# Kernel optimization log

Hardware: AMD Instinct MI355X
Metric: run time of the kernel (lower is better)

Reference implementation:

```python
import jax, jax.numpy as jnp
import numpy as np

S, B, DIM = 1024, 4, 768
N_EXPERTS = 8
# hidden_dim = 256 * ceil(int(2*4*dim/3)/256) = 2048 for dim=768
HID = 2048


def setup_inputs() -> dict:
    key = jax.random.key(0)
    ks = jax.random.split(key, 6)
    scale = 0.02
    return {
        "hidden_states": jax.random.normal(ks[0], (S, B, DIM), dtype=jnp.float32),
        "router_w": jax.random.normal(ks[1], (DIM, N_EXPERTS), dtype=jnp.float32) * scale,
        "router_b": jnp.zeros((N_EXPERTS,), dtype=jnp.float32),
        "w1": jax.random.normal(ks[2], (N_EXPERTS, DIM, HID), dtype=jnp.float32) * scale,
        "w2": jax.random.normal(ks[3], (N_EXPERTS, DIM, HID), dtype=jnp.float32) * scale,
        "w3": jax.random.normal(ks[4], (N_EXPERTS, HID, DIM), dtype=jnp.float32) * scale,
    }


def reference(hidden_states, router_w, router_b, w1, w2, w3):
    s, b, h = hidden_states.shape
    # top-1 router
    route = jax.nn.softmax(hidden_states @ router_w + router_b, axis=2)  # [s,b,E]
    max_prob = jnp.max(route, axis=2).reshape(-1, 1)   # [T,1]
    max_ind = jnp.argmax(route, axis=2).reshape(-1)    # [T]
    x = hidden_states.reshape(-1, h)                   # [T,d]

    out = jnp.zeros_like(x)
    # fixed small loop over experts; masked dispatch (tokens not routed to e
    # are zeroed so they contribute nothing)
    for e in range(N_EXPERTS):
        mask = (max_ind == e)[:, None]                 # [T,1]
        xe = jnp.where(mask, x, 0.0)
        oe = (jax.nn.silu(xe @ w1[e]) * (xe @ w2[e])) @ w3[e]
        out = out + jnp.where(mask, oe, 0.0)

    # original stores expert outputs in a bf16 buffer before the prob combine
    out = out.astype(jnp.bfloat16) * max_prob          # bf16 * f32 -> f32
    return out.reshape(s, b, h)
```

## Files before the change

kernel.cpp:

```cpp
#include <hip/hip_runtime.h>


#define T_TOK 4096
#define DIM   768
#define HID   2048
#define NE    8
#define ECAP  1024

#define KB1 24
#define NB1 128
#define KB2 64
#define NB2 48
#define MBC 64

typedef _Float16 f16x8 __attribute__((ext_vector_type(8)));
typedef float    f32x4 __attribute__((ext_vector_type(4)));

__device__ __forceinline__ float bf16_rne(float v) {
    unsigned u = __float_as_uint(v);
    unsigned r = (u + 0x7fffu + ((u >> 16) & 1u)) & 0xffff0000u;
    return __uint_as_float(r);
}

__global__ void moe_init_kernel(int* __restrict__ counts) {
    if (threadIdx.x < NE) counts[threadIdx.x] = 0;
}

__device__ __forceinline__ void convert_tile(
    const float* __restrict__ src, _Float16* __restrict__ dst,
    float* Lt, int N, int KBc, int ngrp, int kgrp)
{
    const int t  = threadIdx.x;
    const int c4 = (t & 31) * 4;
    const int r0 = (t >> 5) * 8;
    const float* p = src + (size_t)(kgrp * 64 + r0) * N + ngrp * 128 + c4;
    float4 v[8];
#pragma unroll
    for (int j = 0; j < 8; ++j) v[j] = *(const float4*)(p + (size_t)j * N);
#pragma unroll
    for (int j = 0; j < 8; ++j) {
        float* row = &Lt[(r0 + j) * 130 + c4];
        *(float2*)(row)     = make_float2(v[j].x, v[j].y);
        *(float2*)(row + 2) = make_float2(v[j].z, v[j].w);
    }
    __syncthreads();

    const int l = t & 63, w = t >> 6;
    const int fr = l & 15, fq = l >> 4;
#pragma unroll
    for (int i = 0; i < 4; ++i) {
        const int cell = w * 4 + i;
        const int kbl = cell >> 3, nbl = cell & 7;
        f16x8 h;
#pragma unroll
        for (int j = 0; j < 8; ++j)
            h[j] = (_Float16)Lt[(kbl * 32 + fq * 8 + j) * 130 + nbl * 16 + fr];
        const int nb = ngrp * 8 + nbl, kb = kgrp * 2 + kbl;
        *(f16x8*)(dst + ((size_t)nb * KBc + kb) * 512 + l * 8) = h;
    }
}

__global__ __launch_bounds__(256) void moe_convert_w1_kernel(
    const float* __restrict__ w1, _Float16* __restrict__ w1s)
{
    __shared__ float Lt[64 * 130];
    const int e = blockIdx.x / 192, tile = blockIdx.x % 192;
    convert_tile(w1 + (size_t)e * DIM * HID, w1s + (size_t)e * NB1 * KB1 * 512,
                 Lt, HID, KB1, tile & 15, tile >> 4);
}

__global__ __launch_bounds__(256) void moe_convert_w2_kernel(
    const float* __restrict__ w2, _Float16* __restrict__ w2s)
{
    __shared__ float Lt[64 * 130];
    const int e = blockIdx.x / 192, tile = blockIdx.x % 192;
    convert_tile(w2 + (size_t)e * DIM * HID, w2s + (size_t)e * NB1 * KB1 * 512,
                 Lt, HID, KB1, tile & 15, tile >> 4);
}

__global__ __launch_bounds__(256) void moe_convert_w3_kernel(
    const float* __restrict__ w3, _Float16* __restrict__ w3s)
{
    __shared__ float Lt[64 * 130];
    const int e = blockIdx.x / 192, tile = blockIdx.x % 192;
    convert_tile(w3 + (size_t)e * HID * DIM, w3s + (size_t)e * NB2 * KB2 * 512,
                 Lt, DIM, KB2, tile % 6, tile / 6);
}

__global__ __launch_bounds__(256) void moe_router_kernel(
    const float* __restrict__ X, const float* __restrict__ rw,
    const float* __restrict__ rb, float* __restrict__ probs,
    int* __restrict__ counts, int* __restrict__ lists)
{
    const int t    = blockIdx.x * 4 + (threadIdx.x >> 6);
    const int lane = threadIdx.x & 63;
    const float* x = X + (size_t)t * DIM;

    float xv[12];
#pragma unroll
    for (int j = 0; j < 12; ++j) xv[j] = x[lane + j * 64];

    double lg[NE];
#pragma unroll
    for (int e = 0; e < NE; ++e) {
        double s = 0.0;
#pragma unroll
        for (int j = 0; j < 12; ++j)
            s += (double)xv[j] * (double)rw[(lane + j * 64) * NE + e];
#pragma unroll
        for (int off = 32; off >= 1; off >>= 1) s += __shfl_xor(s, off, 64);
        lg[e] = s + (double)rb[e];
    }

    if (lane == 0) {
        double m = lg[0]; int mi = 0;
#pragma unroll
        for (int e = 1; e < NE; ++e)
            if (lg[e] > m) { m = lg[e]; mi = e; }
        float sum = 0.f;
#pragma unroll
        for (int e = 0; e < NE; ++e) sum += expf((float)(lg[e] - m));
        probs[t] = 1.0f / sum;
        int pos = atomicAdd(&counts[mi], 1);
        lists[mi * T_TOK + pos] = t;
    }
}

__global__ __launch_bounds__(256) void moe_gather_kernel(
    const float* __restrict__ X, const int* __restrict__ lists,
    const int* __restrict__ counts, _Float16* __restrict__ Ag)
{
    const int e = blockIdx.z;
    int cnt = counts[e]; if (cnt > ECAP) cnt = ECAP;
    const int mgrp = blockIdx.y;
    if (mgrp * 64 >= ((cnt + 63) & ~63)) return;
    const int t = threadIdx.x, w = t >> 6, l = t & 63;
    const int mb = mgrp * 4 + w;
    const int m  = mb * 16 + (l & 15);
    const bool valid = (m < cnt);
    const int tok = valid ? lists[e * T_TOK + m] : 0;
    const float* xr = X + (size_t)tok * DIM + (l >> 4) * 8;
#pragma unroll
    for (int i = 0; i < 4; ++i) {
        const int kb = blockIdx.x * 4 + i;
        float4 a = make_float4(0.f, 0.f, 0.f, 0.f), b = a;
        if (valid) {
            a = *(const float4*)(xr + kb * 32);
            b = *(const float4*)(xr + kb * 32 + 4);
        }
        f16x8 h;
        h[0] = (_Float16)a.x; h[1] = (_Float16)a.y; h[2] = (_Float16)a.z; h[3] = (_Float16)a.w;
        h[4] = (_Float16)b.x; h[5] = (_Float16)b.y; h[6] = (_Float16)b.z; h[7] = (_Float16)b.w;
        *(f16x8*)(Ag + ((size_t)(e * MBC + mb) * KB1 + kb) * 512 + l * 8) = h;
    }
}

__global__ __launch_bounds__(256, 3) void moe_gemm1_kernel(
    const _Float16* __restrict__ Ag, const _Float16* __restrict__ w1s,
    const _Float16* __restrict__ w2s, const int* __restrict__ counts,
    _Float16* __restrict__ Hs)
{
    const int e = blockIdx.z;
    int cnt = counts[e]; if (cnt > ECAP) cnt = ECAP;
    const int by = blockIdx.y, bx = blockIdx.x;
    if (by * 128 >= cnt) return;
    const int t = threadIdx.x, w = t >> 6, l = t & 63;
    const int wm = w & 1, wn = w >> 1;

    __shared__ _Float16 Ls[2][16 * 512];
    __shared__ _Float16 Ep[4][64 * 40];

    const int c0s = w * 4;
    const _Float16* gsrc[4];
#pragma unroll
    for (int i = 0; i < 4; ++i) {
        const int c = c0s + i;
        if (c < 8)
            gsrc[i] = Ag  + ((size_t)((e * MBC + by * 8 + c) * KB1)) * 512;
        else if (c < 12)
            gsrc[i] = w1s + ((size_t)((e * NB1 + bx * 4 + (c - 8)) * KB1)) * 512;
        else
            gsrc[i] = w2s + ((size_t)((e * NB1 + bx * 4 + (c - 12)) * KB1)) * 512;
        gsrc[i] += (size_t)l * 8;
    }

    f32x4 acc1[4][2], acc2[4][2];
    const f32x4 zero = {0.f, 0.f, 0.f, 0.f};
#pragma unroll
    for (int i = 0; i < 4; ++i)
#pragma unroll
        for (int j = 0; j < 2; ++j) { acc1[i][j] = zero; acc2[i][j] = zero; }

    f16x8 st[4];
    auto G = [&](int kb) {
#pragma unroll
        for (int i = 0; i < 4; ++i)
            st[i] = *(const f16x8*)(gsrc[i] + (size_t)kb * 512);
    };

    G(0);
    for (int kb = 0; kb < KB1; ++kb) {
        _Float16* Lb = &Ls[kb & 1][0];
#pragma unroll
        for (int i = 0; i < 4; ++i)
            *(f16x8*)(Lb + (c0s + i) * 512 + l * 8) = st[i];
        __syncthreads();
        if (kb + 1 < KB1) G(kb + 1);

        f16x8 a[4], p[2], q[2];
#pragma unroll
        for (int i = 0; i < 4; ++i)
            a[i] = *(const f16x8*)(Lb + (wm * 4 + i) * 512 + l * 8);
#pragma unroll
        for (int j = 0; j < 2; ++j) {
            p[j] = *(const f16x8*)(Lb + (8  + wn * 2 + j) * 512 + l * 8);
            q[j] = *(const f16x8*)(Lb + (12 + wn * 2 + j) * 512 + l * 8);
        }
#pragma unroll
        for (int i = 0; i < 4; ++i)
#pragma unroll
            for (int j = 0; j < 2; ++j) {
                acc1[i][j] = __builtin_amdgcn_mfma_f32_16x16x32_f16(a[i], p[j], acc1[i][j], 0, 0, 0);
                acc2[i][j] = __builtin_amdgcn_mfma_f32_16x16x32_f16(a[i], q[j], acc2[i][j], 0, 0, 0);
            }
    }

    const int fq = l >> 4, fr = l & 15;
#pragma unroll
    for (int i = 0; i < 4; ++i)
#pragma unroll
        for (int j = 0; j < 2; ++j)
#pragma unroll
            for (int r = 0; r < 4; ++r) {
                const float h1 = acc1[i][j][r], h2 = acc2[i][j][r];
                const float s  = h1 / (1.f + __expf(-h1)) * h2;
                Ep[w][(i * 16 + fq * 4 + r) * 40 + j * 16 + fr] = (_Float16)s;
            }
    __syncthreads();
    const int kbH = bx * 2 + wn;
#pragma unroll
    for (int i = 0; i < 4; ++i) {
        f16x8 v = *(const f16x8*)&Ep[w][(i * 16 + fr) * 40 + fq * 8];
        *(f16x8*)(Hs + ((size_t)((e * MBC + by * 8 + wm * 4 + i) * KB2 + kbH)) * 512 + l * 8) = v;
    }
}

__global__ __launch_bounds__(256, 3) void moe_gemm2_kernel(
    const _Float16* __restrict__ Hs, const _Float16* __restrict__ w3s,
    const int* __restrict__ lists, const int* __restrict__ counts,
    const float* __restrict__ probs, float* __restrict__ out)
{
    const int e = blockIdx.z;
    int cnt = counts[e]; if (cnt > ECAP) cnt = ECAP;
    const int by = blockIdx.y, bx = blockIdx.x;
    if (by * 64 >= cnt) return;
    const int t = threadIdx.x, w = t >> 6, l = t & 63;

    __shared__ _Float16 La[2][8 * 512];

    const _Float16* Asrc = Hs + ((size_t)((e * MBC + by * 4 + w) * KB2)) * 512 + l * 8;
    const int nb0 = e * NB2 + bx * 8 + w * 2;
    const _Float16* Bb = w3s + ((size_t)nb0 * KB2) * 512 + l * 8;

    f32x4 acc[4][2];
    const f32x4 zero = {0.f, 0.f, 0.f, 0.f};
#pragma unroll
    for (int i = 0; i < 4; ++i) { acc[i][0] = zero; acc[i][1] = zero; }

    f16x8 stA[2];
    f16x8 vB0[4], vB1[4];

    auto GA = [&](int s) {
        stA[0] = *(const f16x8*)(Asrc + (size_t)(2 * s)     * 512);
        stA[1] = *(const f16x8*)(Asrc + (size_t)(2 * s + 1) * 512);
    };
    auto GB = [&](f16x8* vB, int s) {
#pragma unroll
        for (int u = 0; u < 2; ++u)
#pragma unroll
            for (int j = 0; j < 2; ++j)
                vB[u * 2 + j] = *(const f16x8*)(Bb + ((size_t)(j * KB2 + 2 * s + u)) * 512);
    };
    auto STEP = [&](int s, const f16x8* curB, f16x8* nxtB, _Float16* Lb) {
        *(f16x8*)(Lb +      w  * 512 + l * 8) = stA[0];
        *(f16x8*)(Lb + (4 + w) * 512 + l * 8) = stA[1];
        __syncthreads();
        if (s + 1 < KB2 / 2) { GA(s + 1); GB(nxtB, s + 1); }
#pragma unroll
        for (int u = 0; u < 2; ++u) {
            f16x8 a[4];
#pragma unroll
            for (int i = 0; i < 4; ++i)
                a[i] = *(const f16x8*)(Lb + (u * 4 + i) * 512 + l * 8);
#pragma unroll
            for (int i = 0; i < 4; ++i)
#pragma unroll
                for (int j = 0; j < 2; ++j)
                    acc[i][j] = __builtin_amdgcn_mfma_f32_16x16x32_f16(a[i], curB[u * 2 + j], acc[i][j], 0, 0, 0);
        }
    };

    GA(0); GB(vB0, 0);
    for (int s2 = 0; s2 < KB2 / 2; s2 += 2) {
        STEP(s2,     vB0, vB1, &La[0][0]);
        STEP(s2 + 1, vB1, vB0, &La[1][0]);
    }

    const int* list = lists + e * T_TOK;
    const int fq = l >> 4, fr = l & 15;
    const int c0 = bx * 128 + w * 32;
#pragma unroll
    for (int i = 0; i < 4; ++i)
#pragma unroll
        for (int r = 0; r < 4; ++r) {
            const int m = by * 64 + i * 16 + fq * 4 + r;
            if (m < cnt) {
                const int tok = list[m];
                const float pb = probs[tok];
                float* orow = out + (size_t)tok * DIM + c0 + fr;
                orow[0]  = bf16_rne(acc[i][0][r]) * pb;
                orow[16] = bf16_rne(acc[i][1][r]) * pb;
            }
        }
}

extern "C" void kernel_launch(void* const* d_in, const int* in_sizes, int n_in,
                              void* d_out, int out_size, void* d_ws, size_t ws_size,
                              hipStream_t stream) {
    const float* X  = (const float*)d_in[0];
    const float* rw = (const float*)d_in[1];
    const float* rb = (const float*)d_in[2];
    const float* w1 = (const float*)d_in[3];
    const float* w2 = (const float*)d_in[4];
    const float* w3 = (const float*)d_in[5];
    float* out = (float*)d_out;

    char* ws = (char*)d_ws;
    int*      counts = (int*)(ws + 0);
    int*      lists  = (int*)(ws + 256);
    float*    probs  = (float*)(ws + 131328);
    const size_t WSZ = 25165824;
    _Float16* w1s = (_Float16*)(ws + 147712);
    _Float16* w2s = (_Float16*)(ws + 147712 + WSZ);
    _Float16* w3s = (_Float16*)(ws + 147712 + 2 * WSZ);
    _Float16* Ag  = (_Float16*)(ws + 147712 + 3 * WSZ);
    _Float16* Hs  = (_Float16*)(ws + 147712 + 3 * WSZ + 12582912);

    hipLaunchKernelGGL(moe_init_kernel, dim3(1), dim3(64), 0, stream, counts);
    hipLaunchKernelGGL(moe_convert_w1_kernel, dim3(1536), dim3(256), 0, stream, w1, w1s);
    hipLaunchKernelGGL(moe_convert_w2_kernel, dim3(1536), dim3(256), 0, stream, w2, w2s);
    hipLaunchKernelGGL(moe_convert_w3_kernel, dim3(1536), dim3(256), 0, stream, w3, w3s);
    hipLaunchKernelGGL(moe_router_kernel, dim3(T_TOK / 4), dim3(256), 0, stream,
                       X, rw, rb, probs, counts, lists);
    hipLaunchKernelGGL(moe_gather_kernel, dim3(6, 16, 8), dim3(256), 0, stream,
                       X, lists, counts, Ag);
    hipLaunchKernelGGL(moe_gemm1_kernel, dim3(32, 8, 8), dim3(256), 0, stream,
                       Ag, w1s, w2s, counts, Hs);
    hipLaunchKernelGGL(moe_gemm2_kernel, dim3(6, 16, 8), dim3(256), 0, stream,
                       Hs, w3s, lists, counts, probs, out);
}
```

Before: 328.8 us.

## Split router into per-token argmax and deterministic ballot-based list build

The router now spreads each token's 8 expert dot products across lane groups, using float4 loads and shuffle reductions, and writes only the argmax index and probability. A new per-expert kernel builds token lists in token order using ballot and prefix counts, replacing the atomic append and the separate counts-init kernel. This removes atomic contention and makes list order deterministic, at the cost of one extra launch in which only 8 blocks serially scan all 4096 tokens. maxind reuses the Ag workspace before the gather overwrites it.

```diff
diff --git a/kernel.cpp b/kernel.cpp
--- a/kernel.cpp
+++ b/kernel.cpp
@@ -22,10 +22,6 @@
     return __uint_as_float(r);
 }
 
-__global__ void moe_init_kernel(int* __restrict__ counts) {
-    if (threadIdx.x < NE) counts[threadIdx.x] = 0;
-}
-
 __device__ __forceinline__ void convert_tile(
     const float* __restrict__ src, _Float16* __restrict__ dst,
     float* Lt, int N, int KBc, int ngrp, int kgrp)
@@ -90,40 +86,71 @@
 __global__ __launch_bounds__(256) void moe_router_kernel(
     const float* __restrict__ X, const float* __restrict__ rw,
     const float* __restrict__ rb, float* __restrict__ probs,
-    int* __restrict__ counts, int* __restrict__ lists)
-{
-    const int t    = blockIdx.x * 4 + (threadIdx.x >> 6);
-    const int lane = threadIdx.x & 63;
-    const float* x = X + (size_t)t * DIM;
-
-    float xv[12];
-#pragma unroll
-    for (int j = 0; j < 12; ++j) xv[j] = x[lane + j * 64];
-
-    double lg[NE];
-#pragma unroll
-    for (int e = 0; e < NE; ++e) {
-        double s = 0.0;
-#pragma unroll
-        for (int j = 0; j < 12; ++j)
-            s += (double)xv[j] * (double)rw[(lane + j * 64) * NE + e];
-#pragma unroll
-        for (int off = 32; off >= 1; off >>= 1) s += __shfl_xor(s, off, 64);
-        lg[e] = s + (double)rb[e];
-    }
-
-    if (lane == 0) {
-        double m = lg[0]; int mi = 0;
-#pragma unroll
-        for (int e = 1; e < NE; ++e)
-            if (lg[e] > m) { m = lg[e]; mi = e; }
-        float sum = 0.f;
-#pragma unroll
-        for (int e = 0; e < NE; ++e) sum += expf((float)(lg[e] - m));
-        probs[t] = 1.0f / sum;
-        int pos = atomicAdd(&counts[mi], 1);
-        lists[mi * T_TOK + pos] = t;
-    }
+    int* __restrict__ maxind)
+{
+    const int t = blockIdx.x * 4 + (threadIdx.x >> 6);
+    const int l = threadIdx.x & 63;
+    const int e = l >> 3;
+    const int g = l & 7;
+    const float* x = X + (size_t)t * DIM + g * 96;
+    const float* w = rw + e;
+
+    double s0 = 0.0, s1 = 0.0;
+#pragma unroll
+    for (int j4 = 0; j4 < 24; ++j4) {
+        const float4 xv = *(const float4*)(x + j4 * 4);
+        const int d = (g * 96 + j4 * 4) * NE;
+        s0 += (double)xv.x * (double)w[d];
+        s1 += (double)xv.y * (double)w[d + NE];
+        s0 += (double)xv.z * (double)w[d + 2 * NE];
+        s1 += (double)xv.w * (double)w[d + 3 * NE];
+    }
+    double s = s0 + s1;
+    s += __shfl_xor(s, 1, 64);
+    s += __shfl_xor(s, 2, 64);
+    s += __shfl_xor(s, 4, 64);
+    s += (double)rb[e];
+
+    double m = s; int mi = e;
+#pragma unroll
+    for (int o = 8; o <= 32; o <<= 1) {
+        const double om = __shfl_xor(m, o, 64);
+        const int   omi = __shfl_xor(mi, o, 64);
+        if (om > m || (om == m && omi < mi)) { m = om; mi = omi; }
+    }
+    float ex = __expf((float)(s - m));
+#pragma unroll
+    for (int o = 8; o <= 32; o <<= 1) ex += __shfl_xor(ex, o, 64);
+
+    if (l == 0) { probs[t] = 1.0f / ex; maxind[t] = mi; }
+}
+
+__global__ __launch_bounds__(256) void moe_lists_kernel(
+    const int* __restrict__ maxind, int* __restrict__ counts,
+    int* __restrict__ lists)
+{
+    const int e = blockIdx.x;
+    const int tid = threadIdx.x, wid = tid >> 6, lane = tid & 63;
+    __shared__ int wsum[4];
+    int* dst = lists + e * T_TOK;
+    int base = 0;
+    for (int t0 = 0; t0 < T_TOK; t0 += 256) {
+        const int t = t0 + tid;
+        const bool pred = (maxind[t] == e);
+        const unsigned long long bal = __ballot(pred);
+        const int prefix = __popcll(bal & ((1ull << lane) - 1ull));
+        if (lane == 0) wsum[wid] = __popcll(bal);
+        __syncthreads();
+        int woff = 0;
+#pragma unroll
+        for (int w2 = 0; w2 < 4; ++w2)
+            if (w2 < wid) woff += wsum[w2];
+        const int tot = wsum[0] + wsum[1] + wsum[2] + wsum[3];
+        if (pred) dst[base + woff + prefix] = t;
+        base += tot;
+        __syncthreads();
+    }
+    if (tid == 0) counts[e] = base;
 }
 
 __global__ __launch_bounds__(256) void moe_gather_kernel(
@@ -345,13 +372,15 @@
     _Float16* w3s = (_Float16*)(ws + 147712 + 2 * WSZ);
     _Float16* Ag  = (_Float16*)(ws + 147712 + 3 * WSZ);
     _Float16* Hs  = (_Float16*)(ws + 147712 + 3 * WSZ + 12582912);
-
-    hipLaunchKernelGGL(moe_init_kernel, dim3(1), dim3(64), 0, stream, counts);
+    int* maxind = (int*)Ag;
+
     hipLaunchKernelGGL(moe_convert_w1_kernel, dim3(1536), dim3(256), 0, stream, w1, w1s);
     hipLaunchKernelGGL(moe_convert_w2_kernel, dim3(1536), dim3(256), 0, stream, w2, w2s);
     hipLaunchKernelGGL(moe_convert_w3_kernel, dim3(1536), dim3(256), 0, stream, w3, w3s);
     hipLaunchKernelGGL(moe_router_kernel, dim3(T_TOK / 4), dim3(256), 0, stream,
-                       X, rw, rb, probs, counts, lists);
+                       X, rw, rb, probs, maxind);
+    hipLaunchKernelGGL(moe_lists_kernel, dim3(NE), dim3(256), 0, stream,
+                       maxind, counts, lists);
     hipLaunchKernelGGL(moe_gather_kernel, dim3(6, 16, 8), dim3(256), 0, stream,
                        X, lists, counts, Ag);
     hipLaunchKernelGGL(moe_gemm1_kernel, dim3(32, 8, 8), dim3(256), 0, stream,
```

New measurement: 314.6 us. 4.3% less time.
